# Optimization experiments

Measured on AMD Instinct MI355X. Metric: run time of the kernel, lower is better.

## Reference

```python
import jax, jax.numpy as jnp
import numpy as np

B, L, V, D = 8, 2048, 1024, 512  # batch, seq (max_len), vocab_size (input feat), embedding_dim

def setup_inputs() -> dict:
    key = jax.random.key(0)
    kx, kq, kk, kv = jax.random.split(key, 4)
    scale = 1.0 / np.sqrt(V)
    return {
        "x": jax.random.normal(kx, (B, L, V), dtype=jnp.float32),
        "Wq": jax.random.uniform(kq, (D, V), dtype=jnp.float32, minval=-scale, maxval=scale),
        "Wk": jax.random.uniform(kk, (D, V), dtype=jnp.float32, minval=-scale, maxval=scale),
        "Wv": jax.random.uniform(kv, (D, V), dtype=jnp.float32, minval=-scale, maxval=scale),
    }

def reference(x, Wq, Wk, Wv):
    # nn.Linear without bias: y = x @ W.T
    q = jnp.einsum('blv,dv->bld', x, Wq)
    k = jnp.einsum('blv,dv->bld', x, Wk)
    v = jnp.einsum('blv,dv->bld', x, Wv)
    scores = jnp.einsum('bqd,bkd->bqk', q, k) / jnp.sqrt(jnp.float32(D))
    attn = jax.nn.softmax(scores, axis=2)
    return jnp.einsum('bqk,bkd->bqd', attn, v)
```

## Files before the change

### kernel.cpp

```cpp
#include <hip/hip_runtime.h>
#include <cstdint>
#include <cstddef>


typedef __attribute__((ext_vector_type(8))) __bf16 bf16x8;
typedef __attribute__((ext_vector_type(16))) float f32x16;
typedef __attribute__((ext_vector_type(4))) unsigned short ushort4v;
typedef __attribute__((ext_vector_type(4))) unsigned int uint4v;

__device__ __forceinline__ unsigned short f2bf(float f) {
  unsigned u = __float_as_uint(f);
  return (unsigned short)((u + 0x7fffu + ((u >> 16) & 1u)) >> 16);
}

__device__ __forceinline__ void async_load16(const unsigned short* g, unsigned short* l) {
  __builtin_amdgcn_global_load_lds(
      (__attribute__((address_space(1))) void*)(g),
      (__attribute__((address_space(3))) void*)(l), 16, 0, 0);
}

__global__ __launch_bounds__(256) void cvt_f32_bf16(const float* __restrict__ src,
                                                    unsigned short* __restrict__ dst) {
  int i = (blockIdx.x * 256 + threadIdx.x) * 4;
  float4 v = *(const float4*)(src + i);
  ushort4v o;
  o.x = f2bf(v.x); o.y = f2bf(v.y); o.z = f2bf(v.z); o.w = f2bf(v.w);
  *(ushort4v*)(dst + i) = o;
}

__global__ __launch_bounds__(256) void cvt_w3(const float* __restrict__ a,
                                              const float* __restrict__ b,
                                              const float* __restrict__ c,
                                              unsigned short* __restrict__ dst) {
  int bx = blockIdx.x;
  const float* src = (bx < 512) ? a : (bx < 1024) ? b : c;
  int seg = (bx < 512) ? 0 : (bx < 1024) ? 1 : 2;
  int i = ((bx & 511) * 256 + threadIdx.x) * 4;
  float4 v = *(const float4*)(src + i);
  ushort4v o;
  o.x = f2bf(v.x); o.y = f2bf(v.y); o.z = f2bf(v.z); o.w = f2bf(v.w);
  *(ushort4v*)(dst + seg * 524288 + i) = o;
}

__global__ __launch_bounds__(256) void gemm_qkv(
    const unsigned short* __restrict__ A,
    const unsigned short* __restrict__ Bw,
    unsigned short* __restrict__ qk,
    unsigned short* __restrict__ vT) {
  __shared__ unsigned short sA[128 * 64];
  __shared__ unsigned short sB[128 * 64];
  const int tid = threadIdx.x;
  const int lane = tid & 63, wid = tid >> 6;
  const int wm = wid & 1, wn = wid >> 1;
  const int l31 = lane & 31, half = lane >> 5;

  A += (size_t)blockIdx.y * 128 * 1024;
  Bw += (size_t)blockIdx.x * 128 * 1024;

  f32x16 acc[2][2] = {};

  for (int k0 = 0; k0 < 1024; k0 += 64) {
    __syncthreads();
    #pragma unroll
    for (int p = 0; p < 4; ++p) {
      int u = p * 256 + tid;
      int r = u >> 3, cs = (u & 7) ^ (r & 7);
      async_load16(&A[(size_t)r * 1024 + k0 + cs * 8], &sA[u * 8]);
      async_load16(&Bw[(size_t)r * 1024 + k0 + cs * 8], &sB[u * 8]);
    }
    __syncthreads();

    #pragma unroll
    for (int ks = 0; ks < 4; ++ks) {
      int cb = ks * 2 + half;
      bf16x8 aF[2], bF[2];
      #pragma unroll
      for (int i = 0; i < 2; ++i) {
        int rA = wm * 64 + i * 32 + l31;
        aF[i] = *(const bf16x8*)&sA[(rA * 8 + (cb ^ (rA & 7))) * 8];
        int rB = wn * 64 + i * 32 + l31;
        bF[i] = *(const bf16x8*)&sB[(rB * 8 + (cb ^ (rB & 7))) * 8];
      }
      #pragma unroll
      for (int mt = 0; mt < 2; ++mt)
        #pragma unroll
        for (int nt = 0; nt < 2; ++nt)
          acc[mt][nt] = __builtin_amdgcn_mfma_f32_32x32x16_bf16(
              aF[mt], bF[nt], acc[mt][nt], 0, 0, 0);
    }
  }

  if (blockIdx.x < 8) {
    unsigned short* Cc = qk + (size_t)blockIdx.y * 128 * 1024 + (size_t)blockIdx.x * 128;
    #pragma unroll
    for (int mt = 0; mt < 2; ++mt)
      #pragma unroll
      for (int nt = 0; nt < 2; ++nt) {
        int col = wn * 64 + nt * 32 + l31;
        #pragma unroll
        for (int q = 0; q < 4; ++q) {
          int row = wm * 64 + mt * 32 + half * 4 + q * 8;
          #pragma unroll
          for (int r2 = 0; r2 < 4; ++r2)
            Cc[(size_t)(row + r2) * 1024 + col] = f2bf(acc[mt][nt][q * 4 + r2]);
        }
      }
  } else {
    int nvx = blockIdx.x - 8;
    #pragma unroll
    for (int mt = 0; mt < 2; ++mt)
      #pragma unroll
      for (int nt = 0; nt < 2; ++nt) {
        int d = nvx * 128 + wn * 64 + nt * 32 + l31;
        #pragma unroll
        for (int q = 0; q < 4; ++q) {
          int grow = blockIdx.y * 128 + wm * 64 + mt * 32 + half * 4 + q * 8;
          int b = grow >> 11, l = grow & 2047;
          ushort4v o;
          o.x = f2bf(acc[mt][nt][q * 4 + 0]); o.y = f2bf(acc[mt][nt][q * 4 + 1]);
          o.z = f2bf(acc[mt][nt][q * 4 + 2]); o.w = f2bf(acc[mt][nt][q * 4 + 3]);
          *(ushort4v*)&vT[(size_t)b * 1048576 + (size_t)d * 2048 + l] = o;
        }
      }
  }
}

__global__ __launch_bounds__(256) void gemm_exp(
    const unsigned short* __restrict__ qk,
    unsigned short* __restrict__ S, float scale) {
  __shared__ unsigned short sA[128 * 64];
  __shared__ unsigned short sB[128 * 64];
  const int tid = threadIdx.x;
  const int lane = tid & 63, wid = tid >> 6;
  const int wm = wid & 1, wn = wid >> 1;
  const int l31 = lane & 31, half = lane >> 5;

  const unsigned short* A  = qk + (size_t)blockIdx.z * 2097152 + (size_t)blockIdx.y * 128 * 1024;
  const unsigned short* Bk = qk + 512 + (size_t)blockIdx.z * 2097152 + (size_t)blockIdx.x * 128 * 1024;

  f32x16 acc[2][2] = {};

  for (int k0 = 0; k0 < 512; k0 += 64) {
    __syncthreads();
    #pragma unroll
    for (int p = 0; p < 4; ++p) {
      int u = p * 256 + tid;
      int r = u >> 3, cs = (u & 7) ^ (r & 7);
      async_load16(&A[(size_t)r * 1024 + k0 + cs * 8], &sA[u * 8]);
      async_load16(&Bk[(size_t)r * 1024 + k0 + cs * 8], &sB[u * 8]);
    }
    __syncthreads();

    #pragma unroll
    for (int ks = 0; ks < 4; ++ks) {
      int cb = ks * 2 + half;
      bf16x8 aF[2], bF[2];
      #pragma unroll
      for (int i = 0; i < 2; ++i) {
        int rA = wm * 64 + i * 32 + l31;
        aF[i] = *(const bf16x8*)&sA[(rA * 8 + (cb ^ (rA & 7))) * 8];
        int rB = wn * 64 + i * 32 + l31;
        bF[i] = *(const bf16x8*)&sB[(rB * 8 + (cb ^ (rB & 7))) * 8];
      }
      #pragma unroll
      for (int mt = 0; mt < 2; ++mt)
        #pragma unroll
        for (int nt = 0; nt < 2; ++nt)
          acc[mt][nt] = __builtin_amdgcn_mfma_f32_32x32x16_bf16(
              aF[mt], bF[nt], acc[mt][nt], 0, 0, 0);
    }
  }

  unsigned short* Cc = S + (size_t)blockIdx.z * 4194304 +
                       (size_t)blockIdx.y * 128 * 2048 + (size_t)blockIdx.x * 128;
  #pragma unroll
  for (int mt = 0; mt < 2; ++mt)
    #pragma unroll
    for (int nt = 0; nt < 2; ++nt) {
      int col = wn * 64 + nt * 32 + l31;
      #pragma unroll
      for (int q = 0; q < 4; ++q) {
        int row = wm * 64 + mt * 32 + half * 4 + q * 8;
        #pragma unroll
        for (int r2 = 0; r2 < 4; ++r2)
          Cc[(size_t)(row + r2) * 2048 + col] =
              f2bf(__expf(acc[mt][nt][q * 4 + r2] * scale));
      }
    }
}

__global__ __launch_bounds__(256) void gemm_pv(
    const unsigned short* __restrict__ P, const unsigned short* __restrict__ vT,
    float* __restrict__ out) {
  __shared__ unsigned short sA[128 * 64];
  __shared__ unsigned short sB[128 * 64];
  __shared__ float rs[128];
  const int tid = threadIdx.x;
  const int lane = tid & 63, wid = tid >> 6;
  const int wm = wid & 1, wn = wid >> 1;
  const int l31 = lane & 31, half = lane >> 5;
  const int b = blockIdx.z;
  const int m0 = blockIdx.y * 128, n0 = blockIdx.x * 128;
  const unsigned short* A = P + (size_t)b * 4194304 + (size_t)m0 * 2048;
  const unsigned short* Bv = vT + (size_t)b * 1048576 + (size_t)n0 * 2048;

  f32x16 acc[2][2] = {};
  float rsum[2] = {0.f, 0.f};

  for (int k0 = 0; k0 < 2048; k0 += 64) {
    __syncthreads();
    #pragma unroll
    for (int p = 0; p < 4; ++p) {
      int u = p * 256 + tid;
      int r = u >> 3, cs = (u & 7) ^ (r & 7);
      async_load16(&A[(size_t)r * 2048 + k0 + cs * 8], &sA[u * 8]);
      async_load16(&Bv[(size_t)r * 2048 + k0 + cs * 8], &sB[u * 8]);
    }
    __syncthreads();

    #pragma unroll
    for (int ks = 0; ks < 4; ++ks) {
      int cb = ks * 2 + half;
      bf16x8 aF[2], bF[2];
      #pragma unroll
      for (int i = 0; i < 2; ++i) {
        int rA = wm * 64 + i * 32 + l31;
        aF[i] = *(const bf16x8*)&sA[(rA * 8 + (cb ^ (rA & 7))) * 8];
        int rB = wn * 64 + i * 32 + l31;
        bF[i] = *(const bf16x8*)&sB[(rB * 8 + (cb ^ (rB & 7))) * 8];
      }
      #pragma unroll
      for (int i = 0; i < 2; ++i) {
        uint4v u = __builtin_bit_cast(uint4v, aF[i]);
        #pragma unroll
        for (int t = 0; t < 4; ++t)
          rsum[i] += __uint_as_float(u[t] << 16) +
                     __uint_as_float(u[t] & 0xffff0000u);
      }
      #pragma unroll
      for (int mt = 0; mt < 2; ++mt)
        #pragma unroll
        for (int nt = 0; nt < 2; ++nt)
          acc[mt][nt] = __builtin_amdgcn_mfma_f32_32x32x16_bf16(
              aF[mt], bF[nt], acc[mt][nt], 0, 0, 0);
    }
  }

  #pragma unroll
  for (int i = 0; i < 2; ++i) {
    rsum[i] += __shfl_xor(rsum[i], 32, 64);
    if (lane < 32) rs[wm * 64 + i * 32 + lane] = rsum[i];
  }
  __syncthreads();

  #pragma unroll
  for (int mt = 0; mt < 2; ++mt) {
    #pragma unroll
    for (int q = 0; q < 4; ++q) {
      int rl = wm * 64 + mt * 32 + half * 4 + q * 8;
      int row = m0 + rl;
      float inv0 = __builtin_amdgcn_rcpf(rs[rl]);
      float inv1 = __builtin_amdgcn_rcpf(rs[rl + 1]);
      float inv2 = __builtin_amdgcn_rcpf(rs[rl + 2]);
      float inv3 = __builtin_amdgcn_rcpf(rs[rl + 3]);
      #pragma unroll
      for (int nt = 0; nt < 2; ++nt) {
        int col = n0 + wn * 64 + nt * 32 + l31;
        float* op = out + ((size_t)b * 2048 + row) * 512 + col;
        op[0]    = acc[mt][nt][q * 4 + 0] * inv0;
        op[512]  = acc[mt][nt][q * 4 + 1] * inv1;
        op[1024] = acc[mt][nt][q * 4 + 2] * inv2;
        op[1536] = acc[mt][nt][q * 4 + 3] * inv3;
      }
    }
  }
}

extern "C" void kernel_launch(void* const* d_in, const int* in_sizes, int n_in,
                              void* d_out, int out_size, void* d_ws, size_t ws_size,
                              hipStream_t stream) {
  const float* x  = (const float*)d_in[0];
  const float* Wq = (const float*)d_in[1];
  const float* Wk = (const float*)d_in[2];
  const float* Wv = (const float*)d_in[3];
  float* out = (float*)d_out;
  char* ws = (char*)d_ws;

  unsigned short* xb = (unsigned short*)ws;
  unsigned short* S  = (unsigned short*)ws;
  unsigned short* wf = (unsigned short*)(ws + 33554432);
  unsigned short* qk = (unsigned short*)(ws + 67108864);
  unsigned short* vT = (unsigned short*)(ws + 100663296);

  const float rsqrtD = 0.044194173824159216f;

  hipLaunchKernelGGL(cvt_f32_bf16, dim3(16384), dim3(256), 0, stream, x, xb);
  hipLaunchKernelGGL(cvt_w3, dim3(1536), dim3(256), 0, stream, Wq, Wk, Wv, wf);

  hipLaunchKernelGGL(gemm_qkv, dim3(12, 128, 1), dim3(256), 0, stream, xb, wf, qk, vT);

  hipLaunchKernelGGL(gemm_exp, dim3(16, 16, 8), dim3(256), 0, stream, qk, S, rsqrtD);

  hipLaunchKernelGGL(gemm_pv, dim3(4, 16, 8), dim3(256), 0, stream, S, vT, out);

  (void)in_sizes; (void)n_in; (void)out_size; (void)ws_size;
}
```

Measured before the change: 266.9 us.

## Use 256x128 tiles with triple-buffered async LDS pipeline and 16x16 MFMA

All three GEMMs now share one core routine: 512-thread blocks compute 256x128 output tiles with 16x16x32 bf16 MFMAs. Tiles are staged into three rotating LDS buffers, prefetched two k-steps ahead, and the code waits with explicit vmcnt instead of a double __syncthreads per step. MFMA issue is raised in priority with s_setprio. This targets exposed global-load latency and the low data reuse of the smaller 128x128 tiles. The cost is about 145KB of dynamic LDS per block, which allows only one block per CU, and there are fewer blocks in the grid.

```diff
diff --git a/kernel.cpp b/kernel.cpp
--- a/kernel.cpp
+++ b/kernel.cpp
@@ -4,7 +4,7 @@
 
 
 typedef __attribute__((ext_vector_type(8))) __bf16 bf16x8;
-typedef __attribute__((ext_vector_type(16))) float f32x16;
+typedef __attribute__((ext_vector_type(4))) float f32x4;
 typedef __attribute__((ext_vector_type(4))) unsigned short ushort4v;
 typedef __attribute__((ext_vector_type(4))) unsigned int uint4v;
 
@@ -42,236 +42,207 @@
   *(ushort4v*)(dst + seg * 524288 + i) = o;
 }
 
-__global__ __launch_bounds__(256) void gemm_qkv(
-    const unsigned short* __restrict__ A,
+__device__ __forceinline__ void stage_tile(
+    const unsigned short* __restrict__ A, const unsigned short* __restrict__ B,
+    size_t ldA, size_t ldB, unsigned short* buf, int tid, int k0) {
+  int r = tid >> 3, c = tid & 7;
+  int cs = (c ^ (r & 7)) * 8;
+  #pragma unroll
+  for (int p = 0; p < 4; ++p)
+    async_load16(&A[(size_t)(p * 64 + r) * ldA + k0 + cs], &buf[(p * 512 + tid) * 8]);
+  unsigned short* bb = buf + 16384;
+  #pragma unroll
+  for (int p = 0; p < 2; ++p)
+    async_load16(&B[(size_t)(p * 64 + r) * ldB + k0 + cs], &bb[(p * 512 + tid) * 8]);
+}
+
+template <int NT, bool RSUM>
+__device__ __forceinline__ void gemm_core(
+    const unsigned short* __restrict__ A, const unsigned short* __restrict__ B,
+    size_t ldA, size_t ldB, unsigned short* smem, int tid,
+    f32x4 (&acc)[4][4], float (&rsum)[4]) {
+  const int lane = tid & 63;
+  const int wid = tid >> 6;
+  const int wm = wid & 3, wn = wid >> 2;
+  const int cl = lane & 15, g = lane >> 4;
+
+  stage_tile(A, B, ldA, ldB, smem + 0 * 24576, tid, 0);
+  stage_tile(A, B, ldA, ldB, smem + 1 * 24576, tid, 64);
+
+  int cur = 0;
+  for (int t = 0; t < NT; ++t) {
+    if (t == NT - 1) asm volatile("s_waitcnt vmcnt(0)" ::: "memory");
+    else             asm volatile("s_waitcnt vmcnt(6)" ::: "memory");
+    __builtin_amdgcn_s_barrier();
+    if (t + 2 < NT) {
+      int nb = cur + 2; if (nb >= 3) nb -= 3;
+      stage_tile(A, B, ldA, ldB, smem + nb * 24576, tid, (t + 2) * 64);
+    }
+    const unsigned short* sA = smem + cur * 24576;
+    const unsigned short* sB = sA + 16384;
+
+    bf16x8 aF[4][2], bF[4][2];
+    #pragma unroll
+    for (int mt = 0; mt < 4; ++mt)
+      #pragma unroll
+      for (int kh = 0; kh < 2; ++kh) {
+        int row = wm * 64 + mt * 16 + cl;
+        int ch = (kh * 4 + g) ^ (row & 7);
+        aF[mt][kh] = *(const bf16x8*)&sA[(row * 8 + ch) * 8];
+      }
+    #pragma unroll
+    for (int nt = 0; nt < 4; ++nt)
+      #pragma unroll
+      for (int kh = 0; kh < 2; ++kh) {
+        int row = wn * 64 + nt * 16 + cl;
+        int ch = (kh * 4 + g) ^ (row & 7);
+        bF[nt][kh] = *(const bf16x8*)&sB[(row * 8 + ch) * 8];
+      }
+
+    if (RSUM) {
+      #pragma unroll
+      for (int mt = 0; mt < 4; ++mt)
+        #pragma unroll
+        for (int kh = 0; kh < 2; ++kh) {
+          uint4v u = __builtin_bit_cast(uint4v, aF[mt][kh]);
+          #pragma unroll
+          for (int q = 0; q < 4; ++q)
+            rsum[mt] += __uint_as_float(u[q] << 16) +
+                        __uint_as_float(u[q] & 0xffff0000u);
+        }
+    }
+
+    __builtin_amdgcn_s_setprio(1);
+    #pragma unroll
+    for (int mt = 0; mt < 4; ++mt)
+      #pragma unroll
+      for (int nt = 0; nt < 4; ++nt)
+        #pragma unroll
+        for (int kh = 0; kh < 2; ++kh)
+          acc[mt][nt] = __builtin_amdgcn_mfma_f32_16x16x32_bf16(
+              aF[mt][kh], bF[nt][kh], acc[mt][nt], 0, 0, 0);
+    __builtin_amdgcn_s_setprio(0);
+
+    cur = (cur == 2) ? 0 : cur + 1;
+  }
+}
+
+__global__ __launch_bounds__(512, 2) void gemm_qkv(
+    const unsigned short* __restrict__ A0,
     const unsigned short* __restrict__ Bw,
     unsigned short* __restrict__ qk,
     unsigned short* __restrict__ vT) {
-  __shared__ unsigned short sA[128 * 64];
-  __shared__ unsigned short sB[128 * 64];
+  extern __shared__ __align__(16) unsigned short smem[];
   const int tid = threadIdx.x;
+  const unsigned short* A = A0 + (size_t)blockIdx.y * 256 * 1024;
+  const unsigned short* B = Bw + (size_t)blockIdx.x * 128 * 1024;
+
+  f32x4 acc[4][4] = {};
+  float rsum[4];
+  gemm_core<16, false>(A, B, 1024, 1024, smem, tid, acc, rsum);
+
   const int lane = tid & 63, wid = tid >> 6;
-  const int wm = wid & 1, wn = wid >> 1;
-  const int l31 = lane & 31, half = lane >> 5;
-
-  A += (size_t)blockIdx.y * 128 * 1024;
-  Bw += (size_t)blockIdx.x * 128 * 1024;
-
-  f32x16 acc[2][2] = {};
-
-  for (int k0 = 0; k0 < 1024; k0 += 64) {
-    __syncthreads();
-    #pragma unroll
-    for (int p = 0; p < 4; ++p) {
-      int u = p * 256 + tid;
-      int r = u >> 3, cs = (u & 7) ^ (r & 7);
-      async_load16(&A[(size_t)r * 1024 + k0 + cs * 8], &sA[u * 8]);
-      async_load16(&Bw[(size_t)r * 1024 + k0 + cs * 8], &sB[u * 8]);
-    }
-    __syncthreads();
-
-    #pragma unroll
-    for (int ks = 0; ks < 4; ++ks) {
-      int cb = ks * 2 + half;
-      bf16x8 aF[2], bF[2];
-      #pragma unroll
-      for (int i = 0; i < 2; ++i) {
-        int rA = wm * 64 + i * 32 + l31;
-        aF[i] = *(const bf16x8*)&sA[(rA * 8 + (cb ^ (rA & 7))) * 8];
-        int rB = wn * 64 + i * 32 + l31;
-        bF[i] = *(const bf16x8*)&sB[(rB * 8 + (cb ^ (rB & 7))) * 8];
-      }
-      #pragma unroll
-      for (int mt = 0; mt < 2; ++mt)
+  const int wm = wid & 3, wn = wid >> 2, cl = lane & 15, g = lane >> 4;
+
+  if (blockIdx.x < 8) {
+    unsigned short* Cc = qk + (size_t)blockIdx.y * 256 * 1024 + (size_t)blockIdx.x * 128;
+    #pragma unroll
+    for (int mt = 0; mt < 4; ++mt)
+      #pragma unroll
+      for (int nt = 0; nt < 4; ++nt) {
+        int col = wn * 64 + nt * 16 + cl;
+        int row0 = wm * 64 + mt * 16 + g * 4;
         #pragma unroll
-        for (int nt = 0; nt < 2; ++nt)
-          acc[mt][nt] = __builtin_amdgcn_mfma_f32_32x32x16_bf16(
-              aF[mt], bF[nt], acc[mt][nt], 0, 0, 0);
-    }
-  }
-
-  if (blockIdx.x < 8) {
-    unsigned short* Cc = qk + (size_t)blockIdx.y * 128 * 1024 + (size_t)blockIdx.x * 128;
-    #pragma unroll
-    for (int mt = 0; mt < 2; ++mt)
-      #pragma unroll
-      for (int nt = 0; nt < 2; ++nt) {
-        int col = wn * 64 + nt * 32 + l31;
-        #pragma unroll
-        for (int q = 0; q < 4; ++q) {
-          int row = wm * 64 + mt * 32 + half * 4 + q * 8;
-          #pragma unroll
-          for (int r2 = 0; r2 < 4; ++r2)
-            Cc[(size_t)(row + r2) * 1024 + col] = f2bf(acc[mt][nt][q * 4 + r2]);
-        }
+        for (int j = 0; j < 4; ++j)
+          Cc[(size_t)(row0 + j) * 1024 + col] = f2bf(acc[mt][nt][j]);
       }
   } else {
     int nvx = blockIdx.x - 8;
     #pragma unroll
-    for (int mt = 0; mt < 2; ++mt)
-      #pragma unroll
-      for (int nt = 0; nt < 2; ++nt) {
-        int d = nvx * 128 + wn * 64 + nt * 32 + l31;
-        #pragma unroll
-        for (int q = 0; q < 4; ++q) {
-          int grow = blockIdx.y * 128 + wm * 64 + mt * 32 + half * 4 + q * 8;
-          int b = grow >> 11, l = grow & 2047;
-          ushort4v o;
-          o.x = f2bf(acc[mt][nt][q * 4 + 0]); o.y = f2bf(acc[mt][nt][q * 4 + 1]);
-          o.z = f2bf(acc[mt][nt][q * 4 + 2]); o.w = f2bf(acc[mt][nt][q * 4 + 3]);
-          *(ushort4v*)&vT[(size_t)b * 1048576 + (size_t)d * 2048 + l] = o;
-        }
-      }
-  }
-}
-
-__global__ __launch_bounds__(256) void gemm_exp(
+    for (int mt = 0; mt < 4; ++mt)
+      #pragma unroll
+      for (int nt = 0; nt < 4; ++nt) {
+        int d = nvx * 128 + wn * 64 + nt * 16 + cl;
+        int grow0 = blockIdx.y * 256 + wm * 64 + mt * 16 + g * 4;
+        int b = grow0 >> 11, l0 = grow0 & 2047;
+        ushort4v o;
+        o.x = f2bf(acc[mt][nt][0]); o.y = f2bf(acc[mt][nt][1]);
+        o.z = f2bf(acc[mt][nt][2]); o.w = f2bf(acc[mt][nt][3]);
+        *(ushort4v*)&vT[(size_t)b * 1048576 + (size_t)d * 2048 + l0] = o;
+      }
+  }
+}
+
+__global__ __launch_bounds__(512, 2) void gemm_exp(
     const unsigned short* __restrict__ qk,
     unsigned short* __restrict__ S, float scale) {
-  __shared__ unsigned short sA[128 * 64];
-  __shared__ unsigned short sB[128 * 64];
+  extern __shared__ __align__(16) unsigned short smem[];
   const int tid = threadIdx.x;
+  const unsigned short* A  = qk + (size_t)blockIdx.z * 2097152 + (size_t)blockIdx.y * 256 * 1024;
+  const unsigned short* Bk = qk + 512 + (size_t)blockIdx.z * 2097152 + (size_t)blockIdx.x * 128 * 1024;
+
+  f32x4 acc[4][4] = {};
+  float rsum[4];
+  gemm_core<8, false>(A, Bk, 1024, 1024, smem, tid, acc, rsum);
+
   const int lane = tid & 63, wid = tid >> 6;
-  const int wm = wid & 1, wn = wid >> 1;
-  const int l31 = lane & 31, half = lane >> 5;
-
-  const unsigned short* A  = qk + (size_t)blockIdx.z * 2097152 + (size_t)blockIdx.y * 128 * 1024;
-  const unsigned short* Bk = qk + 512 + (size_t)blockIdx.z * 2097152 + (size_t)blockIdx.x * 128 * 1024;
-
-  f32x16 acc[2][2] = {};
-
-  for (int k0 = 0; k0 < 512; k0 += 64) {
-    __syncthreads();
-    #pragma unroll
-    for (int p = 0; p < 4; ++p) {
-      int u = p * 256 + tid;
-      int r = u >> 3, cs = (u & 7) ^ (r & 7);
-      async_load16(&A[(size_t)r * 1024 + k0 + cs * 8], &sA[u * 8]);
-      async_load16(&Bk[(size_t)r * 1024 + k0 + cs * 8], &sB[u * 8]);
-    }
-    __syncthreads();
-
-    #pragma unroll
-    for (int ks = 0; ks < 4; ++ks) {
-      int cb = ks * 2 + half;
-      bf16x8 aF[2], bF[2];
-      #pragma unroll
-      for (int i = 0; i < 2; ++i) {
-        int rA = wm * 64 + i * 32 + l31;
-        aF[i] = *(const bf16x8*)&sA[(rA * 8 + (cb ^ (rA & 7))) * 8];
-        int rB = wn * 64 + i * 32 + l31;
-        bF[i] = *(const bf16x8*)&sB[(rB * 8 + (cb ^ (rB & 7))) * 8];
-      }
-      #pragma unroll
-      for (int mt = 0; mt < 2; ++mt)
-        #pragma unroll
-        for (int nt = 0; nt < 2; ++nt)
-          acc[mt][nt] = __builtin_amdgcn_mfma_f32_32x32x16_bf16(
-              aF[mt], bF[nt], acc[mt][nt], 0, 0, 0);
-    }
-  }
+  const int wm = wid & 3, wn = wid >> 2, cl = lane & 15, g = lane >> 4;
 
   unsigned short* Cc = S + (size_t)blockIdx.z * 4194304 +
-                       (size_t)blockIdx.y * 128 * 2048 + (size_t)blockIdx.x * 128;
-  #pragma unroll
-  for (int mt = 0; mt < 2; ++mt)
-    #pragma unroll
-    for (int nt = 0; nt < 2; ++nt) {
-      int col = wn * 64 + nt * 32 + l31;
-      #pragma unroll
-      for (int q = 0; q < 4; ++q) {
-        int row = wm * 64 + mt * 32 + half * 4 + q * 8;
-        #pragma unroll
-        for (int r2 = 0; r2 < 4; ++r2)
-          Cc[(size_t)(row + r2) * 2048 + col] =
-              f2bf(__expf(acc[mt][nt][q * 4 + r2] * scale));
-      }
-    }
-}
-
-__global__ __launch_bounds__(256) void gemm_pv(
+                       (size_t)blockIdx.y * 256 * 2048 + (size_t)blockIdx.x * 128;
+  #pragma unroll
+  for (int mt = 0; mt < 4; ++mt)
+    #pragma unroll
+    for (int nt = 0; nt < 4; ++nt) {
+      int col = wn * 64 + nt * 16 + cl;
+      int row0 = wm * 64 + mt * 16 + g * 4;
+      #pragma unroll
+      for (int j = 0; j < 4; ++j)
+        Cc[(size_t)(row0 + j) * 2048 + col] =
+            f2bf(__expf(acc[mt][nt][j] * scale));
+    }
+}
+
+__global__ __launch_bounds__(512, 2) void gemm_pv(
     const unsigned short* __restrict__ P, const unsigned short* __restrict__ vT,
     float* __restrict__ out) {
-  __shared__ unsigned short sA[128 * 64];
-  __shared__ unsigned short sB[128 * 64];
-  __shared__ float rs[128];
+  extern __shared__ __align__(16) unsigned short smem[];
   const int tid = threadIdx.x;
+  const int b = blockIdx.z;
+  const int m0 = blockIdx.y * 256, n0 = blockIdx.x * 128;
+  const unsigned short* A  = P + (size_t)b * 4194304 + (size_t)m0 * 2048;
+  const unsigned short* Bv = vT + (size_t)b * 1048576 + (size_t)n0 * 2048;
+
+  f32x4 acc[4][4] = {};
+  float rsum[4] = {0.f, 0.f, 0.f, 0.f};
+  gemm_core<32, true>(A, Bv, 2048, 2048, smem, tid, acc, rsum);
+
   const int lane = tid & 63, wid = tid >> 6;
-  const int wm = wid & 1, wn = wid >> 1;
-  const int l31 = lane & 31, half = lane >> 5;
-  const int b = blockIdx.z;
-  const int m0 = blockIdx.y * 128, n0 = blockIdx.x * 128;
-  const unsigned short* A = P + (size_t)b * 4194304 + (size_t)m0 * 2048;
-  const unsigned short* Bv = vT + (size_t)b * 1048576 + (size_t)n0 * 2048;
-
-  f32x16 acc[2][2] = {};
-  float rsum[2] = {0.f, 0.f};
-
-  for (int k0 = 0; k0 < 2048; k0 += 64) {
-    __syncthreads();
-    #pragma unroll
-    for (int p = 0; p < 4; ++p) {
-      int u = p * 256 + tid;
-      int r = u >> 3, cs = (u & 7) ^ (r & 7);
-      async_load16(&A[(size_t)r * 2048 + k0 + cs * 8], &sA[u * 8]);
-      async_load16(&Bv[(size_t)r * 2048 + k0 + cs * 8], &sB[u * 8]);
-    }
-    __syncthreads();
-
-    #pragma unroll
-    for (int ks = 0; ks < 4; ++ks) {
-      int cb = ks * 2 + half;
-      bf16x8 aF[2], bF[2];
-      #pragma unroll
-      for (int i = 0; i < 2; ++i) {
-        int rA = wm * 64 + i * 32 + l31;
-        aF[i] = *(const bf16x8*)&sA[(rA * 8 + (cb ^ (rA & 7))) * 8];
-        int rB = wn * 64 + i * 32 + l31;
-        bF[i] = *(const bf16x8*)&sB[(rB * 8 + (cb ^ (rB & 7))) * 8];
-      }
-      #pragma unroll
-      for (int i = 0; i < 2; ++i) {
-        uint4v u = __builtin_bit_cast(uint4v, aF[i]);
-        #pragma unroll
-        for (int t = 0; t < 4; ++t)
-          rsum[i] += __uint_as_float(u[t] << 16) +
-                     __uint_as_float(u[t] & 0xffff0000u);
-      }
-      #pragma unroll
-      for (int mt = 0; mt < 2; ++mt)
-        #pragma unroll
-        for (int nt = 0; nt < 2; ++nt)
-          acc[mt][nt] = __builtin_amdgcn_mfma_f32_32x32x16_bf16(
-              aF[mt], bF[nt], acc[mt][nt], 0, 0, 0);
-    }
-  }
-
-  #pragma unroll
-  for (int i = 0; i < 2; ++i) {
-    rsum[i] += __shfl_xor(rsum[i], 32, 64);
-    if (lane < 32) rs[wm * 64 + i * 32 + lane] = rsum[i];
+  const int wm = wid & 3, wn = wid >> 2, cl = lane & 15, g = lane >> 4;
+
+  float* rs = (float*)(smem + 73728);
+  #pragma unroll
+  for (int mt = 0; mt < 4; ++mt) {
+    float v = rsum[mt];
+    v += __shfl_xor(v, 16, 64);
+    v += __shfl_xor(v, 32, 64);
+    if (wn == 0 && lane < 16) rs[wm * 64 + mt * 16 + lane] = v;
   }
   __syncthreads();
 
   #pragma unroll
-  for (int mt = 0; mt < 2; ++mt) {
-    #pragma unroll
-    for (int q = 0; q < 4; ++q) {
-      int rl = wm * 64 + mt * 32 + half * 4 + q * 8;
-      int row = m0 + rl;
-      float inv0 = __builtin_amdgcn_rcpf(rs[rl]);
-      float inv1 = __builtin_amdgcn_rcpf(rs[rl + 1]);
-      float inv2 = __builtin_amdgcn_rcpf(rs[rl + 2]);
-      float inv3 = __builtin_amdgcn_rcpf(rs[rl + 3]);
-      #pragma unroll
-      for (int nt = 0; nt < 2; ++nt) {
-        int col = n0 + wn * 64 + nt * 32 + l31;
-        float* op = out + ((size_t)b * 2048 + row) * 512 + col;
-        op[0]    = acc[mt][nt][q * 4 + 0] * inv0;
-        op[512]  = acc[mt][nt][q * 4 + 1] * inv1;
-        op[1024] = acc[mt][nt][q * 4 + 2] * inv2;
-        op[1536] = acc[mt][nt][q * 4 + 3] * inv3;
-      }
+  for (int mt = 0; mt < 4; ++mt) {
+    int row0l = wm * 64 + mt * 16 + g * 4;
+    float inv[4];
+    #pragma unroll
+    for (int j = 0; j < 4; ++j) inv[j] = __builtin_amdgcn_rcpf(rs[row0l + j]);
+    #pragma unroll
+    for (int nt = 0; nt < 4; ++nt) {
+      int col = n0 + wn * 64 + nt * 16 + cl;
+      float* op = out + ((size_t)b * 2048 + m0 + row0l) * 512 + col;
+      #pragma unroll
+      for (int j = 0; j < 4; ++j)
+        op[(size_t)j * 512] = acc[mt][nt][j] * inv[j];
     }
   }
 }
@@ -294,14 +265,28 @@
 
   const float rsqrtD = 0.044194173824159216f;
 
+  static bool inited = false;
+  if (!inited) {
+    hipFuncSetAttribute((const void*)gemm_qkv,
+                        hipFuncAttributeMaxDynamicSharedMemorySize, 148480);
+    hipFuncSetAttribute((const void*)gemm_exp,
+                        hipFuncAttributeMaxDynamicSharedMemorySize, 148480);
+    hipFuncSetAttribute((const void*)gemm_pv,
+                        hipFuncAttributeMaxDynamicSharedMemorySize, 148480);
+    inited = true;
+  }
+
   hipLaunchKernelGGL(cvt_f32_bf16, dim3(16384), dim3(256), 0, stream, x, xb);
   hipLaunchKernelGGL(cvt_w3, dim3(1536), dim3(256), 0, stream, Wq, Wk, Wv, wf);
 
-  hipLaunchKernelGGL(gemm_qkv, dim3(12, 128, 1), dim3(256), 0, stream, xb, wf, qk, vT);
-
-  hipLaunchKernelGGL(gemm_exp, dim3(16, 16, 8), dim3(256), 0, stream, qk, S, rsqrtD);
-
-  hipLaunchKernelGGL(gemm_pv, dim3(4, 16, 8), dim3(256), 0, stream, S, vT, out);
+  hipLaunchKernelGGL(gemm_qkv, dim3(12, 64, 1), dim3(512), 147456, stream,
+                     xb, wf, qk, vT);
+
+  hipLaunchKernelGGL(gemm_exp, dim3(16, 8, 8), dim3(512), 147456, stream,
+                     qk, S, rsqrtD);
+
+  hipLaunchKernelGGL(gemm_pv, dim3(4, 8, 8), dim3(512), 148480, stream,
+                     S, vT, out);
 
   (void)in_sizes; (void)n_in; (void)out_size; (void)ws_size;
 }
```

After: 269.1 us. About the same (+0.8%).

## Remap block order for XCD locality and transpose PV GEMM for vectorized stores

Applied to the files above, without the earlier changes.

Block indices in the QKV, QK-exp and PV GEMMs are remapped so that blocks sharing the same batch or row tiles are spread across dispatch slots in a pattern meant to improve L2 locality across chiplets. The PV GEMM is reformulated as V^T·S^T, with the probability matrix as the B operand. Row sums then end up in registers per output row, which removes the shared-memory row-sum exchange and barrier. Outputs are written as float4 along the feature dimension instead of scalar strided stores. The risk is that the remapping interacts poorly with actual hardware dispatch order.

```diff
diff --git a/kernel.cpp b/kernel.cpp
--- a/kernel.cpp
+++ b/kernel.cpp
@@ -43,7 +43,7 @@
 }
 
 __global__ __launch_bounds__(256) void gemm_qkv(
-    const unsigned short* __restrict__ A,
+    const unsigned short* __restrict__ A0,
     const unsigned short* __restrict__ Bw,
     unsigned short* __restrict__ qk,
     unsigned short* __restrict__ vT) {
@@ -54,8 +54,13 @@
   const int wm = wid & 1, wn = wid >> 1;
   const int l31 = lane & 31, half = lane >> 5;
 
-  A += (size_t)blockIdx.y * 128 * 1024;
-  Bw += (size_t)blockIdx.x * 128 * 1024;
+  int flat = blockIdx.x + blockIdx.y * 12;
+  int sub = flat >> 3;
+  int bxp = sub % 12;
+  int byp = (flat & 7) * 16 + sub / 12;
+
+  const unsigned short* A = A0 + (size_t)byp * 128 * 1024;
+  const unsigned short* B = Bw + (size_t)bxp * 128 * 1024;
 
   f32x16 acc[2][2] = {};
 
@@ -66,7 +71,7 @@
       int u = p * 256 + tid;
       int r = u >> 3, cs = (u & 7) ^ (r & 7);
       async_load16(&A[(size_t)r * 1024 + k0 + cs * 8], &sA[u * 8]);
-      async_load16(&Bw[(size_t)r * 1024 + k0 + cs * 8], &sB[u * 8]);
+      async_load16(&B[(size_t)r * 1024 + k0 + cs * 8], &sB[u * 8]);
     }
     __syncthreads();
 
@@ -90,8 +95,8 @@
     }
   }
 
-  if (blockIdx.x < 8) {
-    unsigned short* Cc = qk + (size_t)blockIdx.y * 128 * 1024 + (size_t)blockIdx.x * 128;
+  if (bxp < 8) {
+    unsigned short* Cc = qk + (size_t)byp * 128 * 1024 + (size_t)bxp * 128;
     #pragma unroll
     for (int mt = 0; mt < 2; ++mt)
       #pragma unroll
@@ -106,7 +111,7 @@
         }
       }
   } else {
-    int nvx = blockIdx.x - 8;
+    int nvx = bxp - 8;
     #pragma unroll
     for (int mt = 0; mt < 2; ++mt)
       #pragma unroll
@@ -114,7 +119,7 @@
         int d = nvx * 128 + wn * 64 + nt * 32 + l31;
         #pragma unroll
         for (int q = 0; q < 4; ++q) {
-          int grow = blockIdx.y * 128 + wm * 64 + mt * 32 + half * 4 + q * 8;
+          int grow = byp * 128 + wm * 64 + mt * 32 + half * 4 + q * 8;
           int b = grow >> 11, l = grow & 2047;
           ushort4v o;
           o.x = f2bf(acc[mt][nt][q * 4 + 0]); o.y = f2bf(acc[mt][nt][q * 4 + 1]);
@@ -135,8 +140,12 @@
   const int wm = wid & 1, wn = wid >> 1;
   const int l31 = lane & 31, half = lane >> 5;
 
-  const unsigned short* A  = qk + (size_t)blockIdx.z * 2097152 + (size_t)blockIdx.y * 128 * 1024;
-  const unsigned short* Bk = qk + 512 + (size_t)blockIdx.z * 2097152 + (size_t)blockIdx.x * 128 * 1024;
+  int flat = blockIdx.x + (blockIdx.y << 4) + (blockIdx.z << 8);
+  int z = flat & 7, rem = flat >> 3;
+  int bxp = rem & 15, byp = rem >> 4;
+
+  const unsigned short* A  = qk + (size_t)z * 2097152 + (size_t)byp * 128 * 1024;
+  const unsigned short* Bk = qk + 512 + (size_t)z * 2097152 + (size_t)bxp * 128 * 1024;
 
   f32x16 acc[2][2] = {};
 
@@ -171,8 +180,8 @@
     }
   }
 
-  unsigned short* Cc = S + (size_t)blockIdx.z * 4194304 +
-                       (size_t)blockIdx.y * 128 * 2048 + (size_t)blockIdx.x * 128;
+  unsigned short* Cc = S + (size_t)z * 4194304 +
+                       (size_t)byp * 128 * 2048 + (size_t)bxp * 128;
   #pragma unroll
   for (int mt = 0; mt < 2; ++mt)
     #pragma unroll
@@ -189,20 +198,22 @@
     }
 }
 
-__global__ __launch_bounds__(256) void gemm_pv(
-    const unsigned short* __restrict__ P, const unsigned short* __restrict__ vT,
+__global__ __launch_bounds__(256) void gemm_pvT(
+    const unsigned short* __restrict__ S, const unsigned short* __restrict__ vT,
     float* __restrict__ out) {
   __shared__ unsigned short sA[128 * 64];
   __shared__ unsigned short sB[128 * 64];
-  __shared__ float rs[128];
   const int tid = threadIdx.x;
   const int lane = tid & 63, wid = tid >> 6;
   const int wm = wid & 1, wn = wid >> 1;
   const int l31 = lane & 31, half = lane >> 5;
-  const int b = blockIdx.z;
-  const int m0 = blockIdx.y * 128, n0 = blockIdx.x * 128;
-  const unsigned short* A = P + (size_t)b * 4194304 + (size_t)m0 * 2048;
-  const unsigned short* Bv = vT + (size_t)b * 1048576 + (size_t)n0 * 2048;
+
+  int flat = blockIdx.x + (blockIdx.y << 2) + (blockIdx.z << 6);
+  int b = flat & 7, rem = flat >> 3;
+  int dblk = rem & 3, qblk = rem >> 2;
+
+  const unsigned short* A  = vT + (size_t)b * 1048576 + (size_t)dblk * 128 * 2048;
+  const unsigned short* Bs = S  + (size_t)b * 4194304 + (size_t)qblk * 128 * 2048;
 
   f32x16 acc[2][2] = {};
   float rsum[2] = {0.f, 0.f};
@@ -214,7 +225,7 @@
       int u = p * 256 + tid;
       int r = u >> 3, cs = (u & 7) ^ (r & 7);
       async_load16(&A[(size_t)r * 2048 + k0 + cs * 8], &sA[u * 8]);
-      async_load16(&Bv[(size_t)r * 2048 + k0 + cs * 8], &sB[u * 8]);
+      async_load16(&Bs[(size_t)r * 2048 + k0 + cs * 8], &sB[u * 8]);
     }
     __syncthreads();
 
@@ -231,7 +242,7 @@
       }
       #pragma unroll
       for (int i = 0; i < 2; ++i) {
-        uint4v u = __builtin_bit_cast(uint4v, aF[i]);
+        uint4v u = __builtin_bit_cast(uint4v, bF[i]);
         #pragma unroll
         for (int t = 0; t < 4; ++t)
           rsum[i] += __uint_as_float(u[t] << 16) +
@@ -247,30 +258,24 @@
   }
 
   #pragma unroll
-  for (int i = 0; i < 2; ++i) {
-    rsum[i] += __shfl_xor(rsum[i], 32, 64);
-    if (lane < 32) rs[wm * 64 + i * 32 + lane] = rsum[i];
-  }
-  __syncthreads();
+  for (int i = 0; i < 2; ++i) rsum[i] += __shfl_xor(rsum[i], 32, 64);
 
   #pragma unroll
-  for (int mt = 0; mt < 2; ++mt) {
-    #pragma unroll
-    for (int q = 0; q < 4; ++q) {
-      int rl = wm * 64 + mt * 32 + half * 4 + q * 8;
-      int row = m0 + rl;
-      float inv0 = __builtin_amdgcn_rcpf(rs[rl]);
-      float inv1 = __builtin_amdgcn_rcpf(rs[rl + 1]);
-      float inv2 = __builtin_amdgcn_rcpf(rs[rl + 2]);
-      float inv3 = __builtin_amdgcn_rcpf(rs[rl + 3]);
-      #pragma unroll
-      for (int nt = 0; nt < 2; ++nt) {
-        int col = n0 + wn * 64 + nt * 32 + l31;
-        float* op = out + ((size_t)b * 2048 + row) * 512 + col;
-        op[0]    = acc[mt][nt][q * 4 + 0] * inv0;
-        op[512]  = acc[mt][nt][q * 4 + 1] * inv1;
-        op[1024] = acc[mt][nt][q * 4 + 2] * inv2;
-        op[1536] = acc[mt][nt][q * 4 + 3] * inv3;
+  for (int nt = 0; nt < 2; ++nt) {
+    float inv = __builtin_amdgcn_rcpf(rsum[nt]);
+    int qpos = qblk * 128 + wn * 64 + nt * 32 + l31;
+    #pragma unroll
+    for (int mt = 0; mt < 2; ++mt) {
+      int d0 = dblk * 128 + wm * 64 + mt * 32 + half * 4;
+      float* op = out + ((size_t)b * 2048 + qpos) * 512 + d0;
+      #pragma unroll
+      for (int q = 0; q < 4; ++q) {
+        float4 o;
+        o.x = acc[mt][nt][q * 4 + 0] * inv;
+        o.y = acc[mt][nt][q * 4 + 1] * inv;
+        o.z = acc[mt][nt][q * 4 + 2] * inv;
+        o.w = acc[mt][nt][q * 4 + 3] * inv;
+        *(float4*)(op + q * 8) = o;
       }
     }
   }
@@ -301,7 +306,7 @@
 
   hipLaunchKernelGGL(gemm_exp, dim3(16, 16, 8), dim3(256), 0, stream, qk, S, rsqrtD);
 
-  hipLaunchKernelGGL(gemm_pv, dim3(4, 16, 8), dim3(256), 0, stream, S, vT, out);
+  hipLaunchKernelGGL(gemm_pvT, dim3(4, 16, 8), dim3(256), 0, stream, S, vT, out);
 
   (void)in_sizes; (void)n_in; (void)out_size; (void)ws_size;
 }
```

Result: no change. 267.6 us (+0.3%).
